# Optimization experiments

Hardware: AMD Instinct MI355X
Metric: run time of the kernel (lower is better)

The kernel has to match this reference:

```python
import jax, jax.numpy as jnp
import numpy as np

U, LN, NN, S, W = 160, 512, 400, 16, 64   # units, lines, nodes, scenarios, uncertainties
C_VIOL = 2.0e4
N_ITERS = 500   # fixed PDHG iterations (Chambolle-Pock) for the robust-OPF LP
N_POWER = 30    # power iterations for ||A||


def setup_inputs() -> dict:
    rng = np.random.default_rng(0)
    Pmax = rng.uniform(0.5, 2.0, U).astype(np.float32)
    Cost = rng.uniform(10.0, 50.0, U).astype(np.float32)
    C_r_up = rng.uniform(1.0, 5.0, U).astype(np.float32)
    C_r_down = rng.uniform(1.0, 5.0, U).astype(np.float32)
    PTDF = (0.2 * rng.uniform(-1.0, 1.0, (LN, NN))).astype(np.float32)
    node_G = np.zeros((NN, U), np.float32); node_G[rng.integers(0, NN, U), np.arange(U)] = 1.0
    node_W = np.zeros((NN, W), np.float32); node_W[rng.integers(0, NN, W), np.arange(W)] = 1.0
    node_L = np.eye(NN, dtype=np.float32)
    Pd = rng.uniform(0.0, 1.0, NN).astype(np.float32)
    Pd *= 0.5 * Pmax.sum() / Pd.sum()
    w_exp = rng.uniform(0.1, 0.3, W).astype(np.float32)
    Cap = np.full(LN, 10.0, np.float32)        # generous line capacities
    w_scen = (0.1 * rng.standard_normal((S, W))).astype(np.float32)
    names = ['w_scen','Pmax','Cost','C_r_up','C_r_down','PTDF','node_G','node_W','node_L','Pd','w_exp','Cap']
    vals = [w_scen,Pmax,Cost,C_r_up,C_r_down,PTDF,node_G,node_W,node_L,Pd,w_exp,Cap]
    return {k: jnp.asarray(v) for k, v in zip(names, vals)}


def _solve(w_scen, Pmax, Cost, C_r_up, C_r_down, PTDF, node_G, node_W, node_L, Pd, w_exp, Cap):
    # LP (after eliminating f_margin equalities and the DA_cost epigraph variable):
    #   min Cost@p + C_r_up@ru + C_r_down@rd + c_viol*(sum su + sum sd)
    #   s.t. p+ru<=Pmax ; rd-p<=0 ; |Hg@p + const_flow|<=Cap ; pu<=ru ; pd<=rd
    #        Hg@(pu_s-pd_s)+PTDF@(su-sd)+Hg@p <= Cap-const_flow-Hw@w_s  (and mirrored)
    #        sum(p)=sum(Pd)-sum(w_exp) ; sum(pu_s)-sum(pd_s)+sum(su)-sum(sd)=-sum(w_s)
    # solved with fixed-iteration PDHG; all variables >= 0.
    Hg = PTDF @ node_G            # (LN,U)
    Hw = PTDF @ node_W            # (LN,W)
    const_flow = Hw @ w_exp - PTDF @ (node_L @ Pd)   # (LN,)
    b_ws = Hw @ w_scen.T          # (LN,S)

    def A(x):
        p, ru, rd, pu, pd, su, sd = x
        fp = Hg @ p
        pn = PTDF @ (su - sd)
        scen = Hg @ (pu - pd) + pn[:, None] + fp[:, None]   # (LN,S)
        ineq = (p + ru, rd - p, fp, -fp,
                pu - ru[:, None], pd - rd[:, None], scen, -scen)
        eq = (p.sum(), pu.sum(0) - pd.sum(0) + su.sum() - sd.sum())
        return (ineq, eq)

    def AT(y):
        (y1, y2, y3, y4, y5, y6, y7, y8), (z1, z2) = y
        s78 = y7 - y8              # (LN,S)
        s78s = s78.sum(1)          # (LN,)
        gp = y1 - y2 + Hg.T @ (y3 - y4 + s78s) + z1
        gru = y1 - y5.sum(1)
        grd = y2 - y6.sum(1)
        hgt = Hg.T @ s78           # (U,S)
        gpu = y5 + hgt + z2[None, :]
        gpd = y6 - hgt - z2[None, :]
        pt = PTDF.T @ s78s         # (NN,)
        zs = z2.sum()
        return (gp, gru, grd, gpu, gpd, pt + zs, -pt - zs)

    b_ineq = (Pmax, jnp.zeros(U), Cap - const_flow, Cap + const_flow,
              jnp.zeros((U, S)), jnp.zeros((U, S)),
              (Cap - const_flow)[:, None] - b_ws,
              (Cap + const_flow)[:, None] + b_ws)
    b_eq = (Pd.sum() - w_exp.sum(), -w_scen.sum(1))
    c = (Cost, C_r_up, C_r_down, jnp.zeros((U, S)), jnp.zeros((U, S)),
         C_VIOL * jnp.ones(NN), C_VIOL * jnp.ones(NN))

    tmap = jax.tree_util.tree_map

    def tnorm(t):
        return jnp.sqrt(sum(jnp.vdot(l, l) for l in jax.tree_util.tree_leaves(t)))

    # power iteration for ||A||_2
    v = tmap(jnp.ones_like, c)
    for _ in range(N_POWER):
        v = AT(A(v))
        nv = tnorm(v)
        v = tmap(lambda a: a / nv, v)
    Lop = jax.lax.stop_gradient(jnp.sqrt(tnorm(AT(A(v)))))
    tau = 0.9 / Lop
    sig = 0.9 / Lop

    x0 = tmap(jnp.zeros_like, c)
    y0 = (tmap(jnp.zeros_like, b_ineq), tmap(jnp.zeros_like, b_eq))

    def step(carry, _):
        x, y = carry
        g = tmap(lambda ci, gi: ci + gi, c, AT(y))
        xn = tmap(lambda xi, gi: jnp.maximum(xi - tau * gi, 0.0), x, g)
        xb = tmap(lambda a, b: 2.0 * a - b, xn, x)
        ai, ae = A(xb)
        yi, ye = y
        yin = tmap(lambda yk, ak, bk: jnp.maximum(yk + sig * (ak - bk), 0.0), yi, ai, b_ineq)
        yen = tmap(lambda yk, ak, bk: yk + sig * (ak - bk), ye, ae, b_eq)
        return (xn, (yin, yen)), None

    (x, _), _ = jax.lax.scan(step, (x0, y0), None, length=N_ITERS)
    p, ru, rd, pu, pd, su, sd = x
    flow = Hg @ p + const_flow
    f_up = Cap - flow
    f_down = Cap + flow
    DA_cost = (Cost @ p + C_r_up @ ru + C_r_down @ rd
               + C_VIOL * (su.sum() + sd.sum()))[None]
    return p, ru, rd, pu, pd, f_up, f_down, DA_cost


def reference(w_scen, Pmax, Cost, C_r_up, C_r_down, PTDF, node_G, node_W, node_L, Pd, w_exp, Cap):
    return _solve(w_scen, Pmax, Cost, C_r_up, C_r_down, PTDF, node_G, node_W, node_L, Pd, w_exp, Cap)
```

## Files before the change

kernel.cpp:

```cpp
#include <hip/hip_runtime.h>
#include <math.h>

constexpr int U  = 160;
constexpr int LN = 512;
constexpr int NN = 400;
constexpr int S  = 16;
constexpr int W_ = 64;
constexpr float C_VIOL = 2.0e4f;
constexpr int N_ITERS = 500;
constexpr int N_POWER = 30;

#define WGN 32
#define TPB 512
#define NTH (WGN*TPB)
#define LAUNCH_WGN 256

constexpr int al4(int x){ return (x+3)&~3; }

constexpr int O_HG    = 0;
constexpr int O_HGT   = O_HG   + LN*U;
constexpr int O_PTDFT = O_HGT  + U*LN;
constexpr int O_HW    = O_PTDFT+ NN*LN;
constexpr int O_PDL   = O_HW   + LN*W_;
constexpr int O_CF    = al4(O_PDL + NN);
constexpr int O_B3    = O_CF   + LN;
constexpr int O_B4    = O_B3   + LN;
constexpr int O_BWS   = O_B4   + LN;
constexpr int O_BE1   = O_BWS  + LN*S;
constexpr int O_BE2   = al4(O_BE1 + 1);
constexpr int O_MUT   = al4(O_BE2 + S);
constexpr int O_XBP   = O_MUT;
constexpr int O_XFIN  = O_XBP  + 160;
constexpr int O_DIFF  = O_XFIN + 160;
constexpr int O_SDIFF = O_DIFF + 2560;
constexpr int O_S78   = al4(O_SDIFF+400);
constexpr int O_SW    = O_S78  + 8192;
constexpr int O_Z     = O_SW   + 1024;
constexpr int O_PART  = O_Z    + 20;
constexpr int O_ZEND  = O_PART + 640;
constexpr int O_N2    = O_ZEND;
constexpr int O_EQ1   = O_N2   + 32;
constexpr int O_EQ2   = O_EQ1  + 32;
constexpr int O_EQS   = O_EQ2  + 512;
constexpr int O_ARR   = O_EQS  + 32;
constexpr int O_ELC   = O_ARR  + WGN*16;
constexpr int O_ELT   = O_ELC  + 128;
constexpr int WSF     = O_ELT  + 16;

constexpr int L_SACC = 0;
constexpr int L_P    = al4(L_SACC + 20);
constexpr int L_HG   = al4(L_P + 640);
constexpr int L_HGT  = L_HG + 2560;
constexpr int L_DYN  = al4(L_HGT + 2560);
constexpr int L_XP = L_DYN;
constexpr int L_SD = L_XP + 160;
constexpr int L_DF = L_SD + 400;
constexpr int D_S78T = L_DYN;
constexpr int D_W34  = D_S78T + 16*516;
constexpr int D_S78S = D_W34 + 512;
constexpr int L_TOT  = D_S78S + 512;

__device__ __forceinline__ float wred64(float v){
#pragma unroll
  for (int o = 32; o > 0; o >>= 1) v += __shfl_xor(v, o, 64);
  return v;
}
__device__ __forceinline__ float red16(float v){
  v += __shfl_xor(v, 1, 64); v += __shfl_xor(v, 2, 64);
  v += __shfl_xor(v, 4, 64); v += __shfl_xor(v, 8, 64);
  return v;
}
__device__ __forceinline__ float redchunk(float v){
  v += __shfl_xor(v, 16, 64); v += __shfl_xor(v, 32, 64);
  return v;
}
__device__ __forceinline__ float dot4(float4 a, float4 b){
  return a.x*b.x + a.y*b.y + a.z*b.z + a.w*b.w;
}
__device__ __forceinline__ float ald(const float* p){
  return __hip_atomic_load(p, __ATOMIC_RELAXED, __HIP_MEMORY_SCOPE_AGENT);
}
__device__ __forceinline__ float wgld(const float* p){
  return __hip_atomic_load(p, __ATOMIC_RELAXED, __HIP_MEMORY_SCOPE_WORKGROUP);
}

__global__ void k_zero(float* ws){
  int gt = blockIdx.x*blockDim.x + threadIdx.x;
  int nt = gridDim.x*blockDim.x;
  for (int i = gt; i < WSF - O_MUT; i += nt){
    int a = O_MUT + i;
    float v = 0.f;
    if (a >= O_XBP && a < O_XBP + 160) v = 1.f;
    if (a == O_EQ1) v = (float)U;
    ws[a] = v;
  }
}

__global__ void k_pdl(const float* nL, const float* Pd, float* ws){
  int n = blockIdx.x; int lane = threadIdx.x;
  float p = 0.f;
  for (int m = lane; m < NN; m += 64) p += nL[n*NN+m]*Pd[m];
  p = wred64(p);
  if (lane == 0) ws[O_PDL+n] = p;
}

__global__ void k_hg(const float* PTDF, const float* nG, float* ws){
  int l = blockIdx.x, u = threadIdx.x;
  float acc = 0.f;
  for (int n = 0; n < NN; ++n) acc += PTDF[l*NN+n]*nG[n*U+u];
  ws[O_HG + l*U + u]  = acc;
  ws[O_HGT + u*LN + l] = acc;
}

__global__ void k_hw(const float* PTDF, const float* nW, float* ws){
  int l = blockIdx.x, w = threadIdx.x;
  float acc = 0.f;
  for (int n = 0; n < NN; ++n) acc += PTDF[l*NN+n]*nW[n*W_+w];
  ws[O_HW + l*W_ + w] = acc;
}

__global__ void k_tp(const float* PTDF, float* ws){
  int n = blockIdx.x;
  for (int l = threadIdx.x; l < LN; l += blockDim.x)
    ws[O_PTDFT + n*LN + l] = PTDF[l*NN + n];
}

__global__ void k_misc(const float* PTDF, const float* w_exp, const float* w_scen,
                       const float* Cap, float* ws){
  int l = blockIdx.x; int lane = threadIdx.x;
  float part = ws[O_HW + l*W_ + lane]*w_exp[lane];
  for (int n = lane; n < NN; n += 64) part -= PTDF[l*NN+n]*ws[O_PDL+n];
  float cfv = wred64(part);
  if (lane == 0){
    ws[O_CF+l] = cfv;
    ws[O_B3+l] = Cap[l] - cfv;
    ws[O_B4+l] = Cap[l] + cfv;
  }
  int s = lane & 15, ch = lane >> 4;
  float bp = 0.f;
  for (int w = ch*16; w < ch*16+16; ++w) bp += ws[O_HW + l*W_ + w]*w_scen[s*W_+w];
  bp = redchunk(bp);
  if (lane < 16) ws[O_BWS + l*S + s] = bp;
}

__global__ void k_scal(const float* Pd, const float* w_exp, const float* w_scen, float* ws){
  __shared__ float sr[256];
  int tid = threadIdx.x;
  float p = 0.f;
  for (int i = tid; i < NN; i += 256) p += Pd[i];
  for (int i = tid; i < W_; i += 256) p -= w_exp[i];
  sr[tid] = p; __syncthreads();
  for (int o = 128; o > 0; o >>= 1){ if (tid < o) sr[tid] += sr[tid+o]; __syncthreads(); }
  if (tid == 0) ws[O_BE1] = sr[0];
  if (tid < S){
    float a = 0.f;
    for (int w = 0; w < W_; ++w) a += w_scen[tid*W_+w];
    ws[O_BE2+tid] = -a;
  }
}

extern "C" __global__ void __launch_bounds__(TPB)
k_solver(float* __restrict__ ws, const float* __restrict__ Pmax,
         const float* __restrict__ Cost, const float* __restrict__ Crup,
         const float* __restrict__ Crdn, const float* __restrict__ PTDF,
         const float* __restrict__ Cap, float* __restrict__ out)
{
  const int tid  = threadIdx.x;
  const int lane = tid & 63;
  const int wv   = tid >> 6;
  const int s = lane & 15, ch = lane >> 4;
  unsigned nbar = 0;
  __shared__ __align__(16) float lds[L_TOT];
  __shared__ int s_vb;

  if (tid == 0){
    int xcc;
    asm volatile("s_getreg_b32 %0, hwreg(HW_REG_XCC_ID)" : "=s"(xcc));
    xcc &= 7;
    int* elc = (int*)(ws + O_ELC);
    int* elt = (int*)(ws + O_ELT);
    int rank = __hip_atomic_fetch_add(&elc[xcc*16], 1, __ATOMIC_RELAXED,
                                      __HIP_MEMORY_SCOPE_AGENT);
    __threadfence();
    __hip_atomic_fetch_add(elt, 1, __ATOMIC_RELEASE, __HIP_MEMORY_SCOPE_AGENT);
    while (__hip_atomic_load(elt, __ATOMIC_ACQUIRE, __HIP_MEMORY_SCOPE_AGENT)
           < LAUNCH_WGN)
      __builtin_amdgcn_s_sleep(2);
    __threadfence();
    int best = 0, bc = -1;
    for (int x = 0; x < 8; ++x){
      int c = __hip_atomic_load(&elc[x*16], __ATOMIC_RELAXED,
                                __HIP_MEMORY_SCOPE_AGENT);
      if (c > bc){ bc = c; best = x; }
    }
    s_vb = (xcc == best && rank < WGN) ? rank : -1;
  }
  __syncthreads();
  const int vbid = s_vb;
  if (vbid < 0) return;

  const int gtid = vbid*TPB + tid;

  auto LDC4 = [&](int e)->float4{ return *(const float4*)(ws + e); };
  auto st1  = [&](float* p, float v){ *p = v; };
  auto st2  = [&](float* p, float2 v){ *(float2*)p = v; };

  const bool isU = (wv < 5);
  const int  u   = vbid*5 + wv;
  const int  nw  = vbid*3 + (wv-5);
  const int  NR  = (!isU && nw < 16) ? 5 : 4;

  for (int i = tid; i < 2560; i += TPB) lds[L_HG + i]  = ws[O_HG  + vbid*2560 + i];
  for (int i = tid; i < 2560; i += TPB) lds[L_HGT + i] = ws[O_HGT + vbid*2560 + i];
  __syncthreads();

  float xp=1.f,xru=1.f,xrd=1.f,xpu=1.f,xpd=1.f;
  float ry1=0.f,ry2=0.f,ry5=0.f,ry6=0.f;
  float xsu[5],xsd[5];
  float ly3[2],ly4[2],ly7[2],ly8[2];
  float rz1=0.f, rz2=0.f;
  float tau=0.f, sig=0.f;
#pragma unroll
  for (int r=0;r<5;++r){ xsu[r]=xsd[r]=1.f; }
#pragma unroll
  for (int j=0;j<2;++j){ ly3[j]=ly4[j]=ly7[j]=ly8[j]=0.f; }

  unsigned* arr = (unsigned*)(ws + O_ARR);
  auto gbar = [&](){
    ++nbar;
    asm volatile("s_waitcnt vmcnt(0)" ::: "memory");
    __syncthreads();
    if (tid < WGN){
      if (tid == vbid) *(volatile unsigned*)(arr + vbid*16) = nbar;
      volatile unsigned* f = (volatile unsigned*)(arr + tid*16);
      while (true){
        asm volatile("buffer_inv" ::: "memory");
        asm volatile("s_waitcnt vmcnt(0)" ::: "memory");
        if (*f >= nbar) break;
      }
    }
    __syncthreads();
  };

  auto phaseY = [&](bool pd, int k){
    float scl = 1.f;
    if (!pd && k > 0) scl = 1.f/sqrtf(ald(ws+O_N2+k));
    for (int i = tid; i < 40; i += TPB){ ((float4*)(lds+L_XP))[i] = LDC4(O_XBP+4*i); }
    for (int i = tid; i < 100; i += TPB){ ((float4*)(lds+L_SD))[i] = LDC4(O_SDIFF+4*i); }
    for (int i = tid; i < 640; i += TPB){
      float4 v = LDC4(O_DIFF+4*i);
      int e = 4*i, uu = e >> 4, s0 = e & 15;
      float* d = lds + L_DF + uu*17 + s0;
      d[0]=v.x; d[1]=v.y; d[2]=v.z; d[3]=v.w;
    }
    if (pd && vbid == 0){
      for (int i = tid; i < 160; i += TPB){ ((float4*)(lds+L_P))[i] = LDC4(O_PART+4*i); }
    }
    __syncthreads();

    if (pd && vbid == 0 && wv == 7){
      float acc = 0.f;
      if (lane < 18){
        for (int i = 0; i < WGN; ++i) acc += lds[L_P + i*20 + lane];
      }
      float susd = __shfl(acc, 17, 64);
      float ae1  = __shfl(acc, 16, 64);
      if (lane < 16){
        rz2 += sig*((acc + susd) - ws[O_BE2+lane]);
        st1(ws+O_Z+2+lane, rz2);
      }
      float zst = red16((lane < 16) ? rz2 : 0.f);
      if (lane == 0) st1(ws+O_Z+1, zst);
      if (lane == 16){ rz1 += sig*(ae1 - ws[O_BE1]); st1(ws+O_Z+0, rz1); }
    }

#pragma unroll
    for (int j = 0; j < 2; ++j){
      const int l = vbid*16 + wv*2 + j;
      const float* hgl = lds + L_HG + (wv*2+j)*160;
      float a = hgl[lane]*lds[L_XP+lane] + hgl[lane+64]*lds[L_XP+lane+64];
      if (lane < 32) a += hgl[lane+128]*lds[L_XP+lane+128];
      float fp = wred64(a);
      const float4* pr  = (const float4*)(PTDF + l*NN);
      const float4* sd4 = (const float4*)(lds + L_SD);
      float b = dot4(pr[lane], sd4[lane]);
      if (lane < 36) b += dot4(pr[lane+64], sd4[lane+64]);
      float pn = wred64(b);
      const float* hgc = hgl + ch*40;
      const float* dfc = lds + L_DF + (ch*40)*17 + s;
      float sc = 0.f;
#pragma unroll 8
      for (int i = 0; i < 40; ++i) sc += hgc[i]*dfc[i*17];
      sc = redchunk(sc);
      float scen = sc + fp + pn;
      float b3l = ws[O_B3+l], b4l = ws[O_B4+l];
      float sv;
      if (pd){
        float bw = ws[O_BWS + l*16 + s];
        ly7[j] = fmaxf(ly7[j] + sig*( scen - (b3l - bw)), 0.f);
        ly8[j] = fmaxf(ly8[j] + sig*(-scen - (b4l + bw)), 0.f);
        sv = ly7[j] - ly8[j];
        ly3[j] = fmaxf(ly3[j] + sig*( fp - b3l), 0.f);
        ly4[j] = fmaxf(ly4[j] + sig*(-fp - b4l), 0.f);
      } else {
        sv = 2.f*scen*scl;
        ly3[j] = fp*scl; ly4[j] = -fp*scl;
      }
      if (lane < 16) st1(ws+O_S78 + l*16 + s, sv);
      float ssum = red16(sv);
      if (lane == 0) st2(ws+O_SW + 2*l, make_float2(ly3[j]-ly4[j]+ssum, ssum));
    }
  };

  auto phaseX = [&](bool pd, int k, bool last){
    if (tid < 20) lds[L_SACC+tid] = 0.f;
    for (int i = tid; i < 2048; i += TPB){
      float4 v = LDC4(O_S78+4*i);
      int e = 4*i, ll = e >> 4, s0 = e & 15;
      lds[D_S78T + (s0  )*516 + ll] = v.x;
      lds[D_S78T + (s0+1)*516 + ll] = v.y;
      lds[D_S78T + (s0+2)*516 + ll] = v.z;
      lds[D_S78T + (s0+3)*516 + ll] = v.w;
    }
    for (int i = tid; i < 256; i += TPB){
      float4 v = LDC4(O_SW+4*i);
      lds[D_W34+2*i]  = v.x; lds[D_W34+2*i+1]  = v.z;
      lds[D_S78S+2*i] = v.y; lds[D_S78S+2*i+1] = v.w;
    }
    float scl = 1.f, z1v, z2v, zsv;
    if (pd){
      z1v = wgld(ws+O_Z+0); z2v = ws[O_Z+2+s]; zsv = wgld(ws+O_Z+1);
    } else {
      if (k > 0) scl = 1.f/sqrtf(ald(ws+O_N2+k));
      z1v = ald(ws+O_EQ1+k)*scl;
      z2v = (ald(ws+O_EQ2+k*16+s) + ald(ws+O_EQS+k))*scl;
      zsv = red16(z2v);
    }
    __syncthreads();

    float n2p=0.f, e1p=0.f, a2p=0.f, susdp=0.f, dap=0.f;
    if (isU){
      float y1,y2,y5,y6;
      if (pd){ y1=ry1; y2=ry2; y5=ry5; y6=ry6; }
      else {
        y1=(xp+xru)*scl; y2=(xrd-xp)*scl;
        y5=(xpu-xru)*scl; y6=(xpd-xrd)*scl;
      }
      const float* HT = lds + L_HGT + wv*512;
      const float4* ht4 = (const float4*)HT;
      const float4* w4  = (const float4*)(lds + D_W34);
      float g = dot4(ht4[lane], w4[lane]) + dot4(ht4[lane+64], w4[lane+64]);
      float gdot = wred64(g);
      const float4* sc4f = (const float4*)(lds + D_S78T + s*516);
      float h = 0.f;
#pragma unroll 8
      for (int k2 = 0; k2 < 32; ++k2) h += dot4(ht4[4*k2+ch], sc4f[4*k2+ch]);
      h = redchunk(h);
      float t5 = red16(y5), t6 = red16(y6);
      float gpu = y5 + h + z2v;
      float gpd = y6 - h - z2v;
      float gp  = y1 - y2 + gdot + z1v;
      float gru = y1 - t5;
      float grd = y2 - t6;
      if (pd){
        float xo;
        xo=xp;  xp =fmaxf(xo-tau*(Cost[u]+gp ),0.f); float xbp_=2.f*xp -xo;
        xo=xru; xru=fmaxf(xo-tau*(Crup[u]+gru),0.f); float xbru=2.f*xru-xo;
        xo=xrd; xrd=fmaxf(xo-tau*(Crdn[u]+grd),0.f); float xbrd=2.f*xrd-xo;
        xo=xpu; xpu=fmaxf(xo-tau*gpu,0.f);           float xbpu=2.f*xpu-xo;
        xo=xpd; xpd=fmaxf(xo-tau*gpd,0.f);           float xbpd=2.f*xpd-xo;
        float d = xbpu - xbpd;
        if (lane == 0){ st1(ws+O_XBP+u, xbp_); e1p += xbp_; }
        if (lane < 16){ st1(ws+O_DIFF+u*16+s, d); a2p += d; }
        ry1=fmaxf(y1+sig*(xbp_+xbru-Pmax[u]),0.f);
        ry2=fmaxf(y2+sig*(xbrd-xbp_),0.f);
        ry5=fmaxf(y5+sig*(xbpu-xbru),0.f);
        ry6=fmaxf(y6+sig*(xbpd-xbrd),0.f);
        if (last){
          if (lane == 0){
            st1(ws+O_XFIN+u, xp);
            dap += Cost[u]*xp + Crup[u]*xru + Crdn[u]*xrd;
            out[u]=xp; out[U+u]=xru; out[2*U+u]=xrd;
          }
          if (lane < 16){
            out[3*U + u*16 + s] = xpu;
            out[3*U + U*S + u*16 + s] = xpd;
          }
        }
      } else {
        xp=gp; xru=gru; xrd=grd; xpu=gpu; xpd=gpd;
        float d = gpu - gpd;
        if (lane == 0){ st1(ws+O_XBP+u, gp); e1p += gp; n2p += gp*gp+gru*gru+grd*grd; }
        if (lane < 16){ st1(ws+O_DIFF+u*16+s, d); a2p += d; n2p += gpu*gpu+gpd*gpd; }
      }
    } else {
      const float4* ss4 = (const float4*)(lds + D_S78S);
#pragma unroll
      for (int r = 0; r < 5; ++r){
        if (r >= NR) break;
        int n = nw + 96*r;
        const float* PT = ws + O_PTDFT + n*LN;
        const float4* pt4 = (const float4*)PT;
        float g = dot4(pt4[lane], ss4[lane]) + dot4(pt4[lane+64], ss4[lane+64]);
        float pt = wred64(g);
        if (pd){
          float g1 = C_VIOL + pt + zsv, g2 = C_VIOL - pt - zsv;
          float xo = xsu[r]; xsu[r] = fmaxf(xo - tau*g1, 0.f); float xb1 = 2.f*xsu[r]-xo;
          xo = xsd[r];       xsd[r] = fmaxf(xo - tau*g2, 0.f); float xb2 = 2.f*xsd[r]-xo;
          if (lane == 0){
            st1(ws+O_SDIFF+n, xb1-xb2); susdp += xb1-xb2;
            if (last) dap += C_VIOL*(xsu[r] + xsd[r]);
          }
        } else {
          float gsu = pt + zsv;
          xsu[r] = gsu; xsd[r] = -gsu;
          if (lane == 0){ st1(ws+O_SDIFF+n, 2.f*gsu); susdp += 2.f*gsu; n2p += 2.f*gsu*gsu; }
        }
      }
    }
    float r1 = wred64(e1p);
    float r2 = wred64(susdp);
    float r3 = wred64(n2p + dap);
    if (lane == 0){
      atomicAdd(&lds[L_SACC+16], r1);
      atomicAdd(&lds[L_SACC+17], r2);
      atomicAdd(&lds[L_SACC+18], r3);
    }
    if (lane < 16) atomicAdd(&lds[L_SACC+s], a2p);
    __syncthreads();
    if (pd){
      if (tid < 10)
        st2(ws+O_PART+vbid*20+2*tid, make_float2(lds[L_SACC+2*tid], lds[L_SACC+2*tid+1]));
    } else {
      if (tid < 16) atomicAdd(&ws[O_EQ2+(k+1)*16+tid], lds[L_SACC+tid]);
      else if (tid == 16) atomicAdd(&ws[O_EQ1+k+1], lds[L_SACC+16]);
      else if (tid == 17) atomicAdd(&ws[O_EQS+k+1], lds[L_SACC+17]);
      else if (tid == 18) atomicAdd(&ws[O_N2 +k+1], lds[L_SACC+18]);
    }
  };

  for (int kk = 0; kk <= N_POWER; ++kk){
    phaseY(false, kk); gbar();
    phaseX(false, kk, false); gbar();
  }

  {
    float Lop = sqrtf(sqrtf(ald(ws+O_N2+31)));
    tau = 0.9f/Lop; sig = 0.9f/Lop;
  }

  xp=xru=xrd=xpu=xpd=0.f; ry1=ry2=ry5=ry6=0.f; rz1=rz2=0.f;
#pragma unroll
  for (int r=0;r<5;++r){ xsu[r]=xsd[r]=0.f; }
#pragma unroll
  for (int j=0;j<2;++j){ ly3[j]=ly4[j]=ly7[j]=ly8[j]=0.f; }
  for (int i = gtid; i < O_ZEND - O_MUT; i += NTH) ws[O_MUT+i] = 0.f;
  gbar();

  for (int it = 0; it < N_ITERS; ++it){
    phaseX(true, it, it == N_ITERS-1); gbar();
    if (it < N_ITERS-1){ phaseY(true, it); gbar(); }
  }

  for (int i = tid; i < 40; i += TPB){ ((float4*)(lds+L_XP))[i] = LDC4(O_XFIN+4*i); }
  __syncthreads();
#pragma unroll
  for (int j = 0; j < 2; ++j){
    const int l = vbid*16 + wv*2 + j;
    const float* hgl = lds + L_HG + (wv*2+j)*160;
    float a = hgl[lane]*lds[L_XP+lane] + hgl[lane+64]*lds[L_XP+lane+64];
    if (lane < 32) a += hgl[lane+128]*lds[L_XP+lane+128];
    float flow = wred64(a) + ws[O_CF+l];
    if (lane == 0){
      out[3*U + 2*U*S + l]      = Cap[l] - flow;
      out[3*U + 2*U*S + LN + l] = Cap[l] + flow;
    }
  }
  if (vbid == 0 && wv == 0){
    float da = (lane < WGN) ? ws[O_PART+lane*20+18] : 0.f;
    da = wred64(da);
    if (lane == 0) out[3*U + 2*U*S + 2*LN] = da;
  }
}

extern "C" void kernel_launch(void* const* d_in, const int* in_sizes, int n_in,
                              void* d_out, int out_size, void* d_ws, size_t ws_size,
                              hipStream_t stream){
  const float* w_scen = (const float*)d_in[0];
  const float* Pmax   = (const float*)d_in[1];
  const float* Cost   = (const float*)d_in[2];
  const float* Crup   = (const float*)d_in[3];
  const float* Crdn   = (const float*)d_in[4];
  const float* PTDF   = (const float*)d_in[5];
  const float* nG     = (const float*)d_in[6];
  const float* nW     = (const float*)d_in[7];
  const float* nL     = (const float*)d_in[8];
  const float* Pd     = (const float*)d_in[9];
  const float* w_exp  = (const float*)d_in[10];
  const float* Cap    = (const float*)d_in[11];
  float* ws  = (float*)d_ws;
  float* out = (float*)d_out;

  k_zero<<<dim3(64),  dim3(256), 0, stream>>>(ws);
  k_pdl <<<dim3(NN),  dim3(64),  0, stream>>>(nL, Pd, ws);
  k_hg  <<<dim3(LN),  dim3(U),   0, stream>>>(PTDF, nG, ws);
  k_hw  <<<dim3(LN),  dim3(W_),  0, stream>>>(PTDF, nW, ws);
  k_tp  <<<dim3(NN),  dim3(256), 0, stream>>>(PTDF, ws);
  k_misc<<<dim3(LN),  dim3(64),  0, stream>>>(PTDF, w_exp, w_scen, Cap, ws);
  k_scal<<<dim3(1),   dim3(256), 0, stream>>>(Pd, w_exp, w_scen, ws);
  k_solver<<<dim3(LAUNCH_WGN), dim3(TPB), 0, stream>>>(ws, Pmax, Cost, Crup, Crdn, PTDF, Cap, out);
}
```

Baseline: 4.691 ms.

## Replicate dual reductions per workgroup and store transposed/padded layouts in global workspace

Every workgroup now reads all per-workgroup partial sums, from a double-buffered slot, and reduces them redundantly. This replaces the single-workgroup z update and the global atomics, so z values live in LDS instead of global memory. Scenario and diff arrays are written directly in transposed/padded layout so the LDS staging becomes plain float4 copies. Per-unit constants and b3/b4/bws are also hoisted into registers or LDS, and barrier flags are spaced further apart. The cost is redundant reduction work in each workgroup.

New measurement: 4.784 ms. No clear change (+2.0%).

```diff
diff --git a/kernel.cpp b/kernel.cpp
--- a/kernel.cpp
+++ b/kernel.cpp
@@ -31,32 +31,29 @@
 constexpr int O_MUT   = al4(O_BE2 + S);
 constexpr int O_XBP   = O_MUT;
 constexpr int O_XFIN  = O_XBP  + 160;
-constexpr int O_DIFF  = O_XFIN + 160;
-constexpr int O_SDIFF = O_DIFF + 2560;
-constexpr int O_S78   = al4(O_SDIFF+400);
-constexpr int O_SW    = O_S78  + 8192;
-constexpr int O_Z     = O_SW   + 1024;
-constexpr int O_PART  = O_Z    + 20;
-constexpr int O_ZEND  = O_PART + 640;
-constexpr int O_N2    = O_ZEND;
-constexpr int O_EQ1   = O_N2   + 32;
-constexpr int O_EQ2   = O_EQ1  + 32;
-constexpr int O_EQS   = O_EQ2  + 512;
-constexpr int O_ARR   = O_EQS  + 32;
-constexpr int O_ELC   = O_ARR  + WGN*16;
+constexpr int O_DIFFP = O_XFIN + 160;
+constexpr int O_SDIFF = O_DIFFP+ 2720;
+constexpr int O_S78T  = al4(O_SDIFF+400);
+constexpr int O_SW    = O_S78T + 8256;
+constexpr int O_PARTX = O_SW   + 1024;
+constexpr int O_ARR   = O_PARTX+ 1280;
+constexpr int O_ELC   = O_ARR  + WGN*32;
 constexpr int O_ELT   = O_ELC  + 128;
 constexpr int WSF     = O_ELT  + 16;
 
 constexpr int L_SACC = 0;
-constexpr int L_P    = al4(L_SACC + 20);
+constexpr int L_Z    = 20;
+constexpr int L_P    = 40;
 constexpr int L_HG   = al4(L_P + 640);
 constexpr int L_HGT  = L_HG + 2560;
-constexpr int L_DYN  = al4(L_HGT + 2560);
+constexpr int L_B34  = L_HGT + 2560;
+constexpr int L_BWS2 = L_B34 + 32;
+constexpr int L_DYN  = al4(L_BWS2 + 256);
 constexpr int L_XP = L_DYN;
 constexpr int L_SD = L_XP + 160;
 constexpr int L_DF = L_SD + 400;
 constexpr int D_S78T = L_DYN;
-constexpr int D_W34  = D_S78T + 16*516;
+constexpr int D_W34  = D_S78T + 8256;
 constexpr int D_S78S = D_W34 + 512;
 constexpr int L_TOT  = D_S78S + 512;
 
@@ -76,12 +73,6 @@
 }
 __device__ __forceinline__ float dot4(float4 a, float4 b){
   return a.x*b.x + a.y*b.y + a.z*b.z + a.w*b.w;
-}
-__device__ __forceinline__ float ald(const float* p){
-  return __hip_atomic_load(p, __ATOMIC_RELAXED, __HIP_MEMORY_SCOPE_AGENT);
-}
-__device__ __forceinline__ float wgld(const float* p){
-  return __hip_atomic_load(p, __ATOMIC_RELAXED, __HIP_MEMORY_SCOPE_WORKGROUP);
 }
 
 __global__ void k_zero(float* ws){
@@ -91,7 +82,7 @@
     int a = O_MUT + i;
     float v = 0.f;
     if (a >= O_XBP && a < O_XBP + 160) v = 1.f;
-    if (a == O_EQ1) v = (float)U;
+    if (a == O_PARTX + 640 + 16) v = (float)U;
     ws[a] = v;
   }
 }
@@ -202,8 +193,6 @@
   const int gtid = vbid*TPB + tid;
 
   auto LDC4 = [&](int e)->float4{ return *(const float4*)(ws + e); };
-  auto st1  = [&](float* p, float v){ *p = v; };
-  auto st2  = [&](float* p, float2 v){ *(float2*)p = v; };
 
   const bool isU = (wv < 5);
   const int  u   = vbid*5 + wv;
@@ -212,7 +201,20 @@
 
   for (int i = tid; i < 2560; i += TPB) lds[L_HG + i]  = ws[O_HG  + vbid*2560 + i];
   for (int i = tid; i < 2560; i += TPB) lds[L_HGT + i] = ws[O_HGT + vbid*2560 + i];
+  if (tid < 16){
+    lds[L_B34+2*tid]   = ws[O_B3 + vbid*16 + tid];
+    lds[L_B34+2*tid+1] = ws[O_B4 + vbid*16 + tid];
+  }
+  for (int i = tid; i < 256; i += TPB) lds[L_BWS2+i] = ws[O_BWS + vbid*256 + i];
   __syncthreads();
+
+  float pmax_u=0.f, cost_u=0.f, crup_u=0.f, crdn_u=0.f;
+  if (isU){ pmax_u=Pmax[u]; cost_u=Cost[u]; crup_u=Crup[u]; crdn_u=Crdn[u]; }
+  float be1r=0.f, be2r=0.f;
+  if (wv == 7){
+    if (lane < 16) be2r = ws[O_BE2+lane];
+    if (lane == 16) be1r = ws[O_BE1];
+  }
 
   float xp=1.f,xru=1.f,xrd=1.f,xpu=1.f,xpd=1.f;
   float ry1=0.f,ry2=0.f,ry5=0.f,ry6=0.f;
@@ -231,8 +233,8 @@
     asm volatile("s_waitcnt vmcnt(0)" ::: "memory");
     __syncthreads();
     if (tid < WGN){
-      if (tid == vbid) *(volatile unsigned*)(arr + vbid*16) = nbar;
-      volatile unsigned* f = (volatile unsigned*)(arr + tid*16);
+      if (tid == vbid) *(volatile unsigned*)(arr + vbid*32) = nbar;
+      volatile unsigned* f = (volatile unsigned*)(arr + tid*32);
       while (true){
         asm volatile("buffer_inv" ::: "memory");
         asm volatile("s_waitcnt vmcnt(0)" ::: "memory");
@@ -243,22 +245,21 @@
   };
 
   auto phaseY = [&](bool pd, int k){
+    const int slot = pd ? (k & 1) : ((k-1) & 1);
+    for (int i = tid; i < 40;  i += TPB) ((float4*)(lds+L_XP))[i] = LDC4(O_XBP+4*i);
+    for (int i = tid; i < 100; i += TPB) ((float4*)(lds+L_SD))[i] = LDC4(O_SDIFF+4*i);
+    for (int i = tid; i < 680; i += TPB) ((float4*)(lds+L_DF))[i] = LDC4(O_DIFFP+4*i);
+    for (int i = tid; i < 160; i += TPB) ((float4*)(lds+L_P))[i]  = LDC4(O_PARTX+slot*640+4*i);
+    __syncthreads();
+
     float scl = 1.f;
-    if (!pd && k > 0) scl = 1.f/sqrtf(ald(ws+O_N2+k));
-    for (int i = tid; i < 40; i += TPB){ ((float4*)(lds+L_XP))[i] = LDC4(O_XBP+4*i); }
-    for (int i = tid; i < 100; i += TPB){ ((float4*)(lds+L_SD))[i] = LDC4(O_SDIFF+4*i); }
-    for (int i = tid; i < 640; i += TPB){
-      float4 v = LDC4(O_DIFF+4*i);
-      int e = 4*i, uu = e >> 4, s0 = e & 15;
-      float* d = lds + L_DF + uu*17 + s0;
-      d[0]=v.x; d[1]=v.y; d[2]=v.z; d[3]=v.w;
-    }
-    if (pd && vbid == 0){
-      for (int i = tid; i < 160; i += TPB){ ((float4*)(lds+L_P))[i] = LDC4(O_PART+4*i); }
-    }
-    __syncthreads();
-
-    if (pd && vbid == 0 && wv == 7){
+    if (!pd && k > 0){
+      float a = 0.f;
+      for (int i = 0; i < WGN; ++i) a += lds[L_P + i*20 + 18];
+      scl = 1.f/sqrtf(a);
+    }
+
+    if (pd && wv == 7){
       float acc = 0.f;
       if (lane < 18){
         for (int i = 0; i < WGN; ++i) acc += lds[L_P + i*20 + lane];
@@ -266,18 +267,19 @@
       float susd = __shfl(acc, 17, 64);
       float ae1  = __shfl(acc, 16, 64);
       if (lane < 16){
-        rz2 += sig*((acc + susd) - ws[O_BE2+lane]);
-        st1(ws+O_Z+2+lane, rz2);
+        rz2 += sig*((acc + susd) - be2r);
+        lds[L_Z+2+lane] = rz2;
       }
       float zst = red16((lane < 16) ? rz2 : 0.f);
-      if (lane == 0) st1(ws+O_Z+1, zst);
-      if (lane == 16){ rz1 += sig*(ae1 - ws[O_BE1]); st1(ws+O_Z+0, rz1); }
+      if (lane == 0) lds[L_Z+1] = zst;
+      if (lane == 16){ rz1 += sig*(ae1 - be1r); lds[L_Z+0] = rz1; }
     }
 
 #pragma unroll
     for (int j = 0; j < 2; ++j){
-      const int l = vbid*16 + wv*2 + j;
-      const float* hgl = lds + L_HG + (wv*2+j)*160;
+      const int li = wv*2 + j;
+      const int l  = vbid*16 + li;
+      const float* hgl = lds + L_HG + li*160;
       float a = hgl[lane]*lds[L_XP+lane] + hgl[lane+64]*lds[L_XP+lane+64];
       if (lane < 32) a += hgl[lane+128]*lds[L_XP+lane+128];
       float fp = wred64(a);
@@ -293,10 +295,10 @@
       for (int i = 0; i < 40; ++i) sc += hgc[i]*dfc[i*17];
       sc = redchunk(sc);
       float scen = sc + fp + pn;
-      float b3l = ws[O_B3+l], b4l = ws[O_B4+l];
+      float b3l = lds[L_B34 + li*2], b4l = lds[L_B34 + li*2 + 1];
       float sv;
       if (pd){
-        float bw = ws[O_BWS + l*16 + s];
+        float bw = lds[L_BWS2 + li*16 + s];
         ly7[j] = fmaxf(ly7[j] + sig*( scen - (b3l - bw)), 0.f);
         ly8[j] = fmaxf(ly8[j] + sig*(-scen - (b4l + bw)), 0.f);
         sv = ly7[j] - ly8[j];
@@ -306,34 +308,36 @@
         sv = 2.f*scen*scl;
         ly3[j] = fp*scl; ly4[j] = -fp*scl;
       }
-      if (lane < 16) st1(ws+O_S78 + l*16 + s, sv);
+      if (lane < 16) ws[O_S78T + s*516 + l] = sv;
       float ssum = red16(sv);
-      if (lane == 0) st2(ws+O_SW + 2*l, make_float2(ly3[j]-ly4[j]+ssum, ssum));
+      if (lane == 0) *(float2*)(ws+O_SW+2*l) = make_float2(ly3[j]-ly4[j]+ssum, ssum);
     }
   };
 
   auto phaseX = [&](bool pd, int k, bool last){
     if (tid < 20) lds[L_SACC+tid] = 0.f;
-    for (int i = tid; i < 2048; i += TPB){
-      float4 v = LDC4(O_S78+4*i);
-      int e = 4*i, ll = e >> 4, s0 = e & 15;
-      lds[D_S78T + (s0  )*516 + ll] = v.x;
-      lds[D_S78T + (s0+1)*516 + ll] = v.y;
-      lds[D_S78T + (s0+2)*516 + ll] = v.z;
-      lds[D_S78T + (s0+3)*516 + ll] = v.w;
-    }
-    for (int i = tid; i < 256; i += TPB){
+    for (int i = tid; i < 2064; i += TPB) ((float4*)(lds+D_S78T))[i] = LDC4(O_S78T+4*i);
+    for (int i = tid; i < 128; i += TPB){
       float4 v = LDC4(O_SW+4*i);
       lds[D_W34+2*i]  = v.x; lds[D_W34+2*i+1]  = v.z;
       lds[D_S78S+2*i] = v.y; lds[D_S78S+2*i+1] = v.w;
     }
     float scl = 1.f, z1v, z2v, zsv;
     if (pd){
-      z1v = wgld(ws+O_Z+0); z2v = ws[O_Z+2+s]; zsv = wgld(ws+O_Z+1);
+      z1v = lds[L_Z+0]; z2v = lds[L_Z+2+s]; zsv = lds[L_Z+1];
     } else {
-      if (k > 0) scl = 1.f/sqrtf(ald(ws+O_N2+k));
-      z1v = ald(ws+O_EQ1+k)*scl;
-      z2v = (ald(ws+O_EQ2+k*16+s) + ald(ws+O_EQS+k))*scl;
+      float acc = 0.f;
+      for (int i = 0; i < WGN; ++i) acc += lds[L_P + i*20 + s];
+      float acc3 = 0.f;
+      if (lane < 3){
+        for (int i = 0; i < WGN; ++i) acc3 += lds[L_P + i*20 + 16 + lane];
+      }
+      float z1raw = __shfl(acc3, 0, 64);
+      float eqs   = __shfl(acc3, 1, 64);
+      float n2    = __shfl(acc3, 2, 64);
+      scl = (k > 0) ? 1.f/sqrtf(n2) : 1.f;
+      z1v = z1raw*scl;
+      z2v = (acc + eqs)*scl;
       zsv = red16(z2v);
     }
     __syncthreads();
@@ -364,22 +368,22 @@
       float grd = y2 - t6;
       if (pd){
         float xo;
-        xo=xp;  xp =fmaxf(xo-tau*(Cost[u]+gp ),0.f); float xbp_=2.f*xp -xo;
-        xo=xru; xru=fmaxf(xo-tau*(Crup[u]+gru),0.f); float xbru=2.f*xru-xo;
-        xo=xrd; xrd=fmaxf(xo-tau*(Crdn[u]+grd),0.f); float xbrd=2.f*xrd-xo;
-        xo=xpu; xpu=fmaxf(xo-tau*gpu,0.f);           float xbpu=2.f*xpu-xo;
-        xo=xpd; xpd=fmaxf(xo-tau*gpd,0.f);           float xbpd=2.f*xpd-xo;
+        xo=xp;  xp =fmaxf(xo-tau*(cost_u+gp ),0.f); float xbp_=2.f*xp -xo;
+        xo=xru; xru=fmaxf(xo-tau*(crup_u+gru),0.f); float xbru=2.f*xru-xo;
+        xo=xrd; xrd=fmaxf(xo-tau*(crdn_u+grd),0.f); float xbrd=2.f*xrd-xo;
+        xo=xpu; xpu=fmaxf(xo-tau*gpu,0.f);          float xbpu=2.f*xpu-xo;
+        xo=xpd; xpd=fmaxf(xo-tau*gpd,0.f);          float xbpd=2.f*xpd-xo;
         float d = xbpu - xbpd;
-        if (lane == 0){ st1(ws+O_XBP+u, xbp_); e1p += xbp_; }
-        if (lane < 16){ st1(ws+O_DIFF+u*16+s, d); a2p += d; }
-        ry1=fmaxf(y1+sig*(xbp_+xbru-Pmax[u]),0.f);
+        if (lane == 0){ ws[O_XBP+u] = xbp_; e1p += xbp_; }
+        if (lane < 16){ ws[O_DIFFP+u*17+s] = d; a2p += d; }
+        ry1=fmaxf(y1+sig*(xbp_+xbru-pmax_u),0.f);
         ry2=fmaxf(y2+sig*(xbrd-xbp_),0.f);
         ry5=fmaxf(y5+sig*(xbpu-xbru),0.f);
         ry6=fmaxf(y6+sig*(xbpd-xbrd),0.f);
         if (last){
           if (lane == 0){
-            st1(ws+O_XFIN+u, xp);
-            dap += Cost[u]*xp + Crup[u]*xru + Crdn[u]*xrd;
+            ws[O_XFIN+u] = xp;
+            dap += cost_u*xp + crup_u*xru + crdn_u*xrd;
             out[u]=xp; out[U+u]=xru; out[2*U+u]=xrd;
           }
           if (lane < 16){
@@ -390,8 +394,8 @@
       } else {
         xp=gp; xru=gru; xrd=grd; xpu=gpu; xpd=gpd;
         float d = gpu - gpd;
-        if (lane == 0){ st1(ws+O_XBP+u, gp); e1p += gp; n2p += gp*gp+gru*gru+grd*grd; }
-        if (lane < 16){ st1(ws+O_DIFF+u*16+s, d); a2p += d; n2p += gpu*gpu+gpd*gpd; }
+        if (lane == 0){ ws[O_XBP+u] = gp; e1p += gp; n2p += gp*gp+gru*gru+grd*grd; }
+        if (lane < 16){ ws[O_DIFFP+u*17+s] = d; a2p += d; n2p += gpu*gpu+gpd*gpd; }
       }
     } else {
       const float4* ss4 = (const float4*)(lds + D_S78S);
@@ -408,13 +412,13 @@
           float xo = xsu[r]; xsu[r] = fmaxf(xo - tau*g1, 0.f); float xb1 = 2.f*xsu[r]-xo;
           xo = xsd[r];       xsd[r] = fmaxf(xo - tau*g2, 0.f); float xb2 = 2.f*xsd[r]-xo;
           if (lane == 0){
-            st1(ws+O_SDIFF+n, xb1-xb2); susdp += xb1-xb2;
+            ws[O_SDIFF+n] = xb1-xb2; susdp += xb1-xb2;
             if (last) dap += C_VIOL*(xsu[r] + xsd[r]);
           }
         } else {
           float gsu = pt + zsv;
           xsu[r] = gsu; xsd[r] = -gsu;
-          if (lane == 0){ st1(ws+O_SDIFF+n, 2.f*gsu); susdp += 2.f*gsu; n2p += 2.f*gsu*gsu; }
+          if (lane == 0){ ws[O_SDIFF+n] = 2.f*gsu; susdp += 2.f*gsu; n2p += 2.f*gsu*gsu; }
         }
       }
     }
@@ -428,15 +432,9 @@
     }
     if (lane < 16) atomicAdd(&lds[L_SACC+s], a2p);
     __syncthreads();
-    if (pd){
-      if (tid < 10)
-        st2(ws+O_PART+vbid*20+2*tid, make_float2(lds[L_SACC+2*tid], lds[L_SACC+2*tid+1]));
-    } else {
-      if (tid < 16) atomicAdd(&ws[O_EQ2+(k+1)*16+tid], lds[L_SACC+tid]);
-      else if (tid == 16) atomicAdd(&ws[O_EQ1+k+1], lds[L_SACC+16]);
-      else if (tid == 17) atomicAdd(&ws[O_EQS+k+1], lds[L_SACC+17]);
-      else if (tid == 18) atomicAdd(&ws[O_N2 +k+1], lds[L_SACC+18]);
-    }
+    if (tid < 10)
+      *(float2*)(ws + O_PARTX + (k&1)*640 + vbid*20 + 2*tid) =
+        make_float2(lds[L_SACC+2*tid], lds[L_SACC+2*tid+1]);
   };
 
   for (int kk = 0; kk <= N_POWER; ++kk){
@@ -445,7 +443,9 @@
   }
 
   {
-    float Lop = sqrtf(sqrtf(ald(ws+O_N2+31)));
+    float nf = (lane < WGN) ? ws[O_PARTX + lane*20 + 18] : 0.f;
+    nf = wred64(nf);
+    float Lop = sqrtf(sqrtf(nf));
     tau = 0.9f/Lop; sig = 0.9f/Lop;
   }
 
@@ -454,7 +454,8 @@
   for (int r=0;r<5;++r){ xsu[r]=xsd[r]=0.f; }
 #pragma unroll
   for (int j=0;j<2;++j){ ly3[j]=ly4[j]=ly7[j]=ly8[j]=0.f; }
-  for (int i = gtid; i < O_ZEND - O_MUT; i += NTH) ws[O_MUT+i] = 0.f;
+  for (int i = gtid; i < O_PARTX - O_MUT; i += NTH) ws[O_MUT+i] = 0.f;
+  if (tid < 20) lds[L_Z+tid] = 0.f;
   gbar();
 
   for (int it = 0; it < N_ITERS; ++it){
@@ -462,12 +463,13 @@
     if (it < N_ITERS-1){ phaseY(true, it); gbar(); }
   }
 
-  for (int i = tid; i < 40; i += TPB){ ((float4*)(lds+L_XP))[i] = LDC4(O_XFIN+4*i); }
+  for (int i = tid; i < 40; i += TPB) ((float4*)(lds+L_XP))[i] = LDC4(O_XFIN+4*i);
   __syncthreads();
 #pragma unroll
   for (int j = 0; j < 2; ++j){
-    const int l = vbid*16 + wv*2 + j;
-    const float* hgl = lds + L_HG + (wv*2+j)*160;
+    const int li = wv*2 + j;
+    const int l  = vbid*16 + li;
+    const float* hgl = lds + L_HG + li*160;
     float a = hgl[lane]*lds[L_XP+lane] + hgl[lane+64]*lds[L_XP+lane+64];
     if (lane < 32) a += hgl[lane+128]*lds[L_XP+lane+128];
     float flow = wred64(a) + ws[O_CF+l];
@@ -477,7 +479,7 @@
     }
   }
   if (vbid == 0 && wv == 0){
-    float da = (lane < WGN) ? ws[O_PART+lane*20+18] : 0.f;
+    float da = (lane < WGN) ? ws[O_PARTX + 640 + lane*20 + 18] : 0.f;
     da = wred64(da);
     if (lane == 0) out[3*U + 2*U*S + 2*LN] = da;
   }
```
